# Kernel optimization log

Measured on AMD Instinct MI355X. Metric: run time of the kernel, lower is better.

Reference implementation:

```python
import jax, jax.numpy as jnp
import numpy as np

N, M, D_IN, H1, D, OUT_C = 2048, 128, 352, 512, 256, 13


def _lin_bn_relu(x, w, b, g, be):
    # 1x1 conv == linear over last dim; BN (eval) folded to per-channel affine (g, be)
    return jax.nn.relu(g * (x @ w.T + b) + be)


def _encode(x, wA, bA, gA, beA, wB, bB, gB, beB):
    return _lin_bn_relu(_lin_bn_relu(x, wA, bA, gA, beA), wB, bB, gB, beB)


def setup_inputs() -> dict:
    key = jax.random.key(0)
    ks = iter(jax.random.split(key, 64))

    def wgt(shape, s=0.05):
        return (jax.random.normal(next(ks), shape, jnp.float32) * s)

    def gamma(c):
        return 1.0 + 0.05 * jax.random.normal(next(ks), (c,), jnp.float32)

    inp = {}
    inp['ext_fea'] = jax.random.normal(next(ks), (N, D_IN), jnp.float32)
    inp['lab_fea'] = jax.random.normal(next(ks), (M, D_IN), jnp.float32)
    # convs1: 352->512->256, each Conv1d(1x1)+BN+ReLU
    inp.update(w1a=wgt((H1, D_IN)), b1a=wgt((H1,)), g1a=gamma(H1), be1a=wgt((H1,)))
    inp.update(w1b=wgt((D, H1)), b1b=wgt((D,)), g1b=gamma(D), be1b=wgt((D,)))
    # convs2: same shapes
    inp.update(w2a=wgt((H1, D_IN)), b2a=wgt((H1,)), g2a=gamma(H1), be2a=wgt((H1,)))
    inp.update(w2b=wgt((D, H1)), b2b=wgt((D,)), g2b=gamma(D), be2b=wgt((D,)))
    # wei_conv SharedMLP [256,32,64,256]: three Conv2d(1x1)+BN+ReLU
    inp.update(mw1=wgt((32, D)), mb1=wgt((32,)), mg1=gamma(32), mbe1=wgt((32,)))
    inp.update(mw2=wgt((64, 32)), mb2=wgt((64,)), mg2=gamma(64), mbe2=wgt((64,)))
    inp.update(mw3=wgt((D, 64)), mb3=wgt((D,)), mg3=gamma(D), mbe3=wgt((D,)))
    # fc
    inp.update(fcw=wgt((OUT_C, D)), fcb=wgt((OUT_C,)))
    return inp


def reference(ext_fea, lab_fea,
              w1a, b1a, g1a, be1a, w1b, b1b, g1b, be1b,
              w2a, b2a, g2a, be2a, w2b, b2b, g2b, be2b,
              mw1, mb1, mg1, mbe1, mw2, mb2, mg2, mbe2, mw3, mb3, mg3, mbe3,
              fcw, fcb):
    A = _encode(ext_fea, w1a, b1a, g1a, be1a, w1b, b1b, g1b, be1b)   # [N, 256]
    B = _encode(lab_fea, w2a, b2a, g2a, be2a, w2b, b2b, g2b, be2b)   # [M, 256]
    diff = A[:, None, :] - B[None, :, :]                             # [N, M, 256]
    h = _lin_bn_relu(diff, mw1, mb1, mg1, mbe1)                      # [N, M, 32]
    h = _lin_bn_relu(h, mw2, mb2, mg2, mbe2)                         # [N, M, 64]
    wei = _lin_bn_relu(h, mw3, mb3, mg3, mbe3)                       # [N, M, 256]
    # torch softmax over dim=-1 of [1,256,N,M] == over M == axis 1 here
    wei = jax.nn.softmax(wei, axis=1)
    att = jnp.sum(wei * diff, axis=1)                                # [N, 256]
    return att @ fcw.T + fcb                                         # [N, 13]
```

## Files before the change

### kernel.cpp

```cpp
#include <hip/hip_runtime.h>
#include <stdint.h>


typedef __attribute__((ext_vector_type(4))) float float4_t;
typedef __attribute__((ext_vector_type(4))) float f32x4;
typedef __attribute__((ext_vector_type(8))) short bf16x8;
typedef __attribute__((ext_vector_type(8))) unsigned short ushort8_t;
typedef __attribute__((ext_vector_type(4))) unsigned short ushort4_t;
typedef unsigned short ushort_t;

__device__ __forceinline__ float b2f(unsigned short u) {
  union { unsigned int i; float f; } v; v.i = ((unsigned int)u) << 16; return v.f;
}
__device__ __forceinline__ unsigned short f2b(float f) {
  union { float f; unsigned int i; } v; v.f = f;
  unsigned int x = v.i;
  return (unsigned short)((x + 0x7FFFu + ((x >> 16) & 1u)) >> 16);
}

template<int ISBF>
__device__ __forceinline__ ushort8_t ld8(const void* base, size_t idx) {
  if constexpr (ISBF) {
    return *(const ushort8_t*)((const ushort_t*)base + idx);
  } else {
    const float* p = (const float*)base + idx;
    float4_t v0 = *(const float4_t*)p;
    float4_t v1 = *(const float4_t*)(p + 4);
    ushort8_t u;
    #pragma unroll
    for (int e = 0; e < 4; ++e) { u[e] = f2b(v0[e]); u[4 + e] = f2b(v1[e]); }
    return u;
  }
}

template<int XBF, int WBF, int OUT_BF16>
__global__ __launch_bounds__(256) void enc_mfma(
    const void* __restrict__ XA, const void* __restrict__ WA,
    const float* __restrict__ bA, const float* __restrict__ gA, const float* __restrict__ beA,
    void* __restrict__ YA,
    const void* __restrict__ XB, const void* __restrict__ WB,
    const float* __restrict__ bB, const float* __restrict__ gB, const float* __restrict__ beB,
    void* __restrict__ YB, ushort_t* __restrict__ YBTb,
    int J, int K, int nbxA)
{
  __shared__ ushort_t Xs[2][32][72];
  __shared__ ushort_t Ws[2][32][72];
  const int bx = blockIdx.x, by = blockIdx.y;
  const void* X; const void* W;
  const float *bb, *gg, *bev; void* Y; int i0, isB;
  if (bx < nbxA) { X = XA; W = WA; bb = bA; gg = gA; bev = beA; Y = YA; i0 = bx * 32; isB = 0; }
  else           { X = XB; W = WB; bb = bB; gg = gB; bev = beB; Y = YB; i0 = (bx - nbxA) * 32; isB = 1; }
  const int j0 = by * 32;
  const int tid = threadIdx.x, w = tid >> 6, lane = tid & 63, lg = lane >> 4, lr = lane & 15;
  const int mt = w >> 1, ct = w & 1;
  const int row = tid >> 3, k8 = (tid & 7) * 8;

  f32x4 acc = f32x4{0.f, 0.f, 0.f, 0.f};

  ushort8_t xv = ld8<XBF>(X, (size_t)(i0 + row) * K + k8);
  ushort8_t wv = ld8<WBF>(W, (size_t)(j0 + row) * K + k8);
  for (int kt = 0; kt < K; kt += 64) {
    const int buf = (kt >> 6) & 1;
    *(ushort8_t*)&Xs[buf][row][k8] = xv;
    *(ushort8_t*)&Ws[buf][row][k8] = wv;
    __syncthreads();
    if (kt + 64 < K && kt + 64 + k8 < K) {
      xv = ld8<XBF>(X, (size_t)(i0 + row) * K + kt + 64 + k8);
      wv = ld8<WBF>(W, (size_t)(j0 + row) * K + kt + 64 + k8);
    }
    bf16x8 af0 = *(const bf16x8*)&Xs[buf][mt * 16 + lr][lg * 8];
    bf16x8 bf0 = *(const bf16x8*)&Ws[buf][ct * 16 + lr][lg * 8];
    acc = __builtin_amdgcn_mfma_f32_16x16x32_bf16(af0, bf0, acc, 0, 0, 0);
    if (kt + 32 < K) {
      bf16x8 af1 = *(const bf16x8*)&Xs[buf][mt * 16 + lr][32 + lg * 8];
      bf16x8 bf1 = *(const bf16x8*)&Ws[buf][ct * 16 + lr][32 + lg * 8];
      acc = __builtin_amdgcn_mfma_f32_16x16x32_bf16(af1, bf1, acc, 0, 0, 0);
    }
  }
  const int c = j0 + ct * 16 + lr;
  const float g = gg[c], bv = bb[c], ev = bev[c];
  #pragma unroll
  for (int r = 0; r < 4; ++r) {
    const int rowo = i0 + mt * 16 + 4 * lg + r;
    float t = fmaxf(g * (acc[r] + bv) + ev, 0.f);
    if (OUT_BF16) ((ushort_t*)Y)[(size_t)rowo * J + c] = f2b(t);
    else {
      ((float*)Y)[(size_t)rowo * J + c] = t;
      if (isB && YBTb) YBTb[(size_t)c * 128 + rowo] = f2b(t);
    }
  }
}

__global__ __launch_bounds__(256) void proj32(
    const float* __restrict__ Aenc, const float* __restrict__ Benc,
    const float* __restrict__ mw1, const float* __restrict__ mb1,
    const float* __restrict__ mg1, const float* __restrict__ mbe1,
    float* __restrict__ PA2, float* __restrict__ PB2, int nbxA,
    const float* __restrict__ mw2, const float* __restrict__ mw3,
    ushort_t* __restrict__ mw2b, ushort_t* __restrict__ mw3b)
{
  __shared__ float ps[4][32];
  const int tid = threadIdx.x, bx = blockIdx.x;
  if (bx >= nbxA + 32) {
    const int g = (bx - nbxA - 32) * 256 + tid;
    const float* s; ushort_t* d; int j;
    if (g < 256) { s = mw2; d = mw2b; j = g; }
    else         { s = mw3; d = mw3b; j = g - 256; }
    float4_t v0 = *(const float4_t*)&s[(size_t)j * 8];
    float4_t v1 = *(const float4_t*)&s[(size_t)j * 8 + 4];
    ushort8_t u;
    #pragma unroll
    for (int e = 0; e < 4; ++e) { u[e] = f2b(v0[e]); u[4 + e] = f2b(v1[e]); }
    *(ushort8_t*)&d[(size_t)j * 8] = u;
    return;
  }
  const float* X; float* P; int n0, wb;
  if (bx < nbxA) { X = Aenc; P = PA2; n0 = bx * 4; wb = 1; }
  else           { X = Benc; P = PB2; n0 = (bx - nbxA) * 4; wb = 0; }
  const int k = tid & 31, r = (tid >> 5) & 3, half = tid >> 7;
  const int n = n0 + r;
  const float* xp = &X[(size_t)n * 256 + half * 128];
  const float* wp = &mw1[k * 256 + half * 128];
  float s = 0.f;
  #pragma unroll 8
  for (int q = 0; q < 128; q += 4) {
    float4_t xv = *(const float4_t*)&xp[q];
    float4_t wv = *(const float4_t*)&wp[q];
    #pragma unroll
    for (int e = 0; e < 4; ++e) s = fmaf(xv[e], wv[e], s);
  }
  if (half == 1) ps[r][k] = s;
  __syncthreads();
  if (half == 0) {
    s += ps[r][k];
    P[(size_t)n * 32 + k] = wb ? (mg1[k] * (s + mb1[k]) + mbe1[k]) : (mg1[k] * s);
  }
}

__global__ __launch_bounds__(256, 2) void main_attn(
    const float* __restrict__ PA2, const float* __restrict__ PB2,
    const float* __restrict__ A, const ushort_t* __restrict__ BmTb,
    const ushort_t* __restrict__ mw2b, const float* __restrict__ mb2,
    const float* __restrict__ mg2, const float* __restrict__ mbe2,
    const ushort_t* __restrict__ mw3b, const float* __restrict__ mb3,
    const float* __restrict__ mg3, const float* __restrict__ mbe3,
    const float* __restrict__ fcw, const float* __restrict__ fcb,
    float* __restrict__ outp)
{
  __shared__ __align__(16) char smem[77824];
  const int tid = threadIdx.x;
  const int w = tid >> 6, lane = tid & 63, lg = lane >> 4, lr = lane & 15;
  const int n = blockIdx.x * 4 + w;
  ushort_t* h2s = (ushort_t*)(smem + w * 19456);
  float* attL   = (float*)(smem + w * 19456 + 18432);
  const float LOG2E = 1.4426950408889634f;

  {
    bf16x8 b1[4];
    float g2h[4], b2h[4], e2h[4];
    #pragma unroll
    for (int jt = 0; jt < 4; ++jt) {
      b1[jt] = *(const bf16x8*)&mw2b[(jt * 16 + lr) * 32 + lg * 8];
      const int j = jt * 16 + lr;
      g2h[jt] = mg2[j]; b2h[jt] = mb2[j]; e2h[jt] = mbe2[j];
    }
    const float* pa = &PA2[(size_t)n * 32 + lg * 8];
    float4_t pa0 = *(const float4_t*)pa;
    float4_t pa1 = *(const float4_t*)(pa + 4);
    #pragma unroll
    for (int mt = 0; mt < 8; ++mt) {
      const float* pb = &PB2[(size_t)(mt * 16 + lr) * 32 + lg * 8];
      float4_t pb0 = *(const float4_t*)pb;
      float4_t pb1 = *(const float4_t*)(pb + 4);
      bf16x8 a1;
      #pragma unroll
      for (int e = 0; e < 4; ++e) {
        a1[e]     = (short)f2b(fmaxf(pa0[e] - pb0[e], 0.f));
        a1[4 + e] = (short)f2b(fmaxf(pa1[e] - pb1[e], 0.f));
      }
      f32x4 acc1[4];
      #pragma unroll
      for (int jt = 0; jt < 4; ++jt) acc1[jt] = f32x4{0.f, 0.f, 0.f, 0.f};
      #pragma unroll
      for (int jt = 0; jt < 4; ++jt)
        acc1[jt] = __builtin_amdgcn_mfma_f32_16x16x32_bf16(a1, b1[jt], acc1[jt], 0, 0, 0);
      #pragma unroll
      for (int jt = 0; jt < 4; ++jt)
        #pragma unroll
        for (int r = 0; r < 4; ++r)
          h2s[(mt * 16 + 4 * lg + r) * 72 + jt * 16 + lr] =
              f2b(fmaxf(g2h[jt] * (acc1[jt][r] + b2h[jt]) + e2h[jt], 0.f));
    }
  }

  bf16x8 af0[8], af1[8];
  #pragma unroll
  for (int mt = 0; mt < 8; ++mt) {
    af0[mt] = *(const bf16x8*)&h2s[(mt * 16 + lr) * 72 + lg * 8];
    af1[mt] = *(const bf16x8*)&h2s[(mt * 16 + lr) * 72 + 32 + lg * 8];
  }

  #pragma unroll 4
  for (int ct = 0; ct < 16; ++ct) {
    const int c = ct * 16 + lr;
    bf16x8 bfr0 = *(const bf16x8*)&mw3b[(size_t)c * 64 + lg * 8];
    bf16x8 bfr1 = *(const bf16x8*)&mw3b[(size_t)c * 64 + 32 + lg * 8];
    f32x4 acc[8];
    #pragma unroll
    for (int mt = 0; mt < 8; ++mt) acc[mt] = f32x4{0.f, 0.f, 0.f, 0.f};
    #pragma unroll
    for (int mt = 0; mt < 8; ++mt) {
      acc[mt] = __builtin_amdgcn_mfma_f32_16x16x32_bf16(af0[mt], bfr0, acc[mt], 0, 0, 0);
      acc[mt] = __builtin_amdgcn_mfma_f32_16x16x32_bf16(af1[mt], bfr1, acc[mt], 0, 0, 0);
    }
    const float g = mg3[c];
    const float gs = g * LOG2E;
    const float cs = (g * mb3[c] + mbe3[c]) * LOG2E;
    f32x4 sm4 = f32x4{0.f, 0.f, 0.f, 0.f};
    f32x4 wb4 = f32x4{0.f, 0.f, 0.f, 0.f};
    #pragma unroll
    for (int mt = 0; mt < 8; ++mt) {
      ushort4_t bv4 = *(const ushort4_t*)&BmTb[(size_t)c * 128 + mt * 16 + 4 * lg];
      #pragma unroll
      for (int r = 0; r < 4; ++r) {
        float t = fmaf(gs, acc[mt][r], cs);
        float p = __builtin_amdgcn_exp2f(__builtin_amdgcn_fmed3f(t, 0.f, 80.f));
        sm4[r] += p;
        wb4[r] = fmaf(p, b2f(bv4[r]), wb4[r]);
      }
    }
    float sm = (sm4[0] + sm4[1]) + (sm4[2] + sm4[3]);
    float wb = (wb4[0] + wb4[1]) + (wb4[2] + wb4[3]);
    sm += __shfl_xor(sm, 16, 64);  wb += __shfl_xor(wb, 16, 64);
    sm += __shfl_xor(sm, 32, 64);  wb += __shfl_xor(wb, 32, 64);
    if (lg == 0)
      attL[c] = A[(size_t)n * 256 + c] - wb / sm;
  }

  {
    float4_t av = *(const float4_t*)&attL[lane * 4];
    #pragma unroll
    for (int o = 0; o < 13; ++o) {
      float4_t wv = *(const float4_t*)&fcw[(size_t)o * 256 + lane * 4];
      float s = av[0] * wv[0];
      s = fmaf(av[1], wv[1], s);
      s = fmaf(av[2], wv[2], s);
      s = fmaf(av[3], wv[3], s);
      #pragma unroll
      for (int st = 1; st <= 32; st <<= 1) s += __shfl_xor(s, st, 64);
      if (lane == 0) outp[(size_t)n * 13 + o] = s + fcb[o];
    }
  }
}

extern "C" void kernel_launch(void* const* d_in, const int* in_sizes, int n_in,
                              void* d_out, int out_size, void* d_ws, size_t ws_size,
                              hipStream_t stream)
{
  const float* ext = (const float*)d_in[0];
  const float* lab = (const float*)d_in[1];
  const float* w1a = (const float*)d_in[2];
  const float* b1a = (const float*)d_in[3];
  const float* g1a = (const float*)d_in[4];
  const float* be1a= (const float*)d_in[5];
  const float* w1b = (const float*)d_in[6];
  const float* b1b = (const float*)d_in[7];
  const float* g1b = (const float*)d_in[8];
  const float* be1b= (const float*)d_in[9];
  const float* w2a = (const float*)d_in[10];
  const float* b2a = (const float*)d_in[11];
  const float* g2a = (const float*)d_in[12];
  const float* be2a= (const float*)d_in[13];
  const float* w2b = (const float*)d_in[14];
  const float* b2b = (const float*)d_in[15];
  const float* g2b = (const float*)d_in[16];
  const float* be2b= (const float*)d_in[17];
  const float* mw1 = (const float*)d_in[18];
  const float* mb1 = (const float*)d_in[19];
  const float* mg1 = (const float*)d_in[20];
  const float* mbe1= (const float*)d_in[21];
  const float* mw2 = (const float*)d_in[22];
  const float* mb2 = (const float*)d_in[23];
  const float* mg2 = (const float*)d_in[24];
  const float* mbe2= (const float*)d_in[25];
  const float* mw3 = (const float*)d_in[26];
  const float* mb3 = (const float*)d_in[27];
  const float* mg3 = (const float*)d_in[28];
  const float* mbe3= (const float*)d_in[29];
  const float* fcw = (const float*)d_in[30];
  const float* fcb = (const float*)d_in[31];

  char* ws = (char*)d_ws;
  ushort_t* Y1ab = (ushort_t*)(ws);
  float*    PA2  = (float*)(ws);
  float*    PB2  = (float*)(ws + 262144);
  float*    Aenc = (float*)(ws + (2u << 20));
  char* b5 = ws + (4u << 20);
  ushort_t* mw2b  = (ushort_t*)(b5);
  ushort_t* mw3b  = (ushort_t*)(b5 + 4096);
  ushort_t* Y1bb  = (ushort_t*)(b5 + 36864);
  float*    Benc  = (float*)(b5 + 167936);
  ushort_t* BencTb= (ushort_t*)(b5 + 299008);

  enc_mfma<0, 0, 1><<<dim3(68, 16), 256, 0, stream>>>(
      (const void*)ext, (const void*)w1a, b1a, g1a, be1a, (void*)Y1ab,
      (const void*)lab, (const void*)w2a, b2a, g2a, be2a, (void*)Y1bb,
      (ushort_t*)nullptr, 512, 352, 64);
  enc_mfma<1, 0, 0><<<dim3(68, 8), 256, 0, stream>>>(
      (const void*)Y1ab, (const void*)w1b, b1b, g1b, be1b, (void*)Aenc,
      (const void*)Y1bb, (const void*)w2b, b2b, g2b, be2b, (void*)Benc,
      BencTb, 256, 512, 64);
  proj32<<<553, 256, 0, stream>>>(Aenc, Benc, mw1, mb1, mg1, mbe1, PA2, PB2, 512,
                                  mw2, mw3, mw2b, mw3b);
  main_attn<<<512, 256, 0, stream>>>(PA2, PB2, Aenc, BencTb,
                                     mw2b, mb2, mg2, mbe2, mw3b, mb3, mg3, mbe3,
                                     fcw, fcb, (float*)d_out);
}
```

Measured before the change: 82.47 us.

## Fuse 32-wide projection into second encoder epilogue and drop proj32 kernel

Removes the separate proj32 launch. The mw1 projection is computed in the second encoder kernel's epilogue: each block takes partial dot products over its 32 output channels and accumulates them into zeroed PA2/PB2 buffers with atomicAdd. The bf16 weight conversion moves into extra blocks of the first encoder launch. MFMA priority hints are added in main_attn. The change saves a launch and a reread of Aenc/Benc, but adds a memset, float atomics (nondeterministic summation order) and extra shared memory in the encoder.

Result: slower. 89.40 us (+8.4%).

```diff
diff --git a/kernel.cpp b/kernel.cpp
--- a/kernel.cpp
+++ b/kernel.cpp
@@ -33,7 +33,7 @@
   }
 }
 
-template<int XBF, int WBF, int OUT_BF16>
+template<int XBF, int WBF, int OUT_BF16, int DO_CVT, int DO_PROJ>
 __global__ __launch_bounds__(256) void enc_mfma(
     const void* __restrict__ XA, const void* __restrict__ WA,
     const float* __restrict__ bA, const float* __restrict__ gA, const float* __restrict__ beA,
@@ -41,11 +41,35 @@
     const void* __restrict__ XB, const void* __restrict__ WB,
     const float* __restrict__ bB, const float* __restrict__ gB, const float* __restrict__ beB,
     void* __restrict__ YB, ushort_t* __restrict__ YBTb,
-    int J, int K, int nbxA)
+    int J, int K, int nbxA,
+    const float* __restrict__ mw2, const float* __restrict__ mw3,
+    ushort_t* __restrict__ mw2b, ushort_t* __restrict__ mw3b,
+    const float* __restrict__ mw1, const float* __restrict__ mg1,
+    const float* __restrict__ mb1, const float* __restrict__ mbe1,
+    float* __restrict__ PA2, float* __restrict__ PB2)
 {
   __shared__ ushort_t Xs[2][32][72];
   __shared__ ushort_t Ws[2][32][72];
+  __shared__ float tileT[32][33];
   const int bx = blockIdx.x, by = blockIdx.y;
+
+  if constexpr (DO_CVT) {
+    if (bx >= nbxA + 4) {
+      if (by != 0) return;
+      const int g = (bx - nbxA - 4) * 256 + threadIdx.x;
+      const float* s; ushort_t* d; int j;
+      if (g < 256) { s = mw2; d = mw2b; j = g; }
+      else         { s = mw3; d = mw3b; j = g - 256; }
+      float4_t v0 = *(const float4_t*)&s[(size_t)j * 8];
+      float4_t v1 = *(const float4_t*)&s[(size_t)j * 8 + 4];
+      ushort8_t u;
+      #pragma unroll
+      for (int e = 0; e < 4; ++e) { u[e] = f2b(v0[e]); u[4 + e] = f2b(v1[e]); }
+      *(ushort8_t*)&d[(size_t)j * 8] = u;
+      return;
+    }
+  }
+
   const void* X; const void* W;
   const float *bb, *gg, *bev; void* Y; int i0, isB;
   if (bx < nbxA) { X = XA; W = WA; bb = bA; gg = gA; bev = beA; Y = YA; i0 = bx * 32; isB = 0; }
@@ -79,61 +103,50 @@
   }
   const int c = j0 + ct * 16 + lr;
   const float g = gg[c], bv = bb[c], ev = bev[c];
+  float tv[4];
   #pragma unroll
   for (int r = 0; r < 4; ++r) {
     const int rowo = i0 + mt * 16 + 4 * lg + r;
-    float t = fmaxf(g * (acc[r] + bv) + ev, 0.f);
-    if (OUT_BF16) ((ushort_t*)Y)[(size_t)rowo * J + c] = f2b(t);
+    tv[r] = fmaxf(g * (acc[r] + bv) + ev, 0.f);
+    if (OUT_BF16) ((ushort_t*)Y)[(size_t)rowo * J + c] = f2b(tv[r]);
     else {
-      ((float*)Y)[(size_t)rowo * J + c] = t;
-      if (isB && YBTb) YBTb[(size_t)c * 128 + rowo] = f2b(t);
-    }
-  }
-}
-
-__global__ __launch_bounds__(256) void proj32(
-    const float* __restrict__ Aenc, const float* __restrict__ Benc,
-    const float* __restrict__ mw1, const float* __restrict__ mb1,
-    const float* __restrict__ mg1, const float* __restrict__ mbe1,
-    float* __restrict__ PA2, float* __restrict__ PB2, int nbxA,
-    const float* __restrict__ mw2, const float* __restrict__ mw3,
-    ushort_t* __restrict__ mw2b, ushort_t* __restrict__ mw3b)
-{
-  __shared__ float ps[4][32];
-  const int tid = threadIdx.x, bx = blockIdx.x;
-  if (bx >= nbxA + 32) {
-    const int g = (bx - nbxA - 32) * 256 + tid;
-    const float* s; ushort_t* d; int j;
-    if (g < 256) { s = mw2; d = mw2b; j = g; }
-    else         { s = mw3; d = mw3b; j = g - 256; }
-    float4_t v0 = *(const float4_t*)&s[(size_t)j * 8];
-    float4_t v1 = *(const float4_t*)&s[(size_t)j * 8 + 4];
-    ushort8_t u;
-    #pragma unroll
-    for (int e = 0; e < 4; ++e) { u[e] = f2b(v0[e]); u[4 + e] = f2b(v1[e]); }
-    *(ushort8_t*)&d[(size_t)j * 8] = u;
-    return;
-  }
-  const float* X; float* P; int n0, wb;
-  if (bx < nbxA) { X = Aenc; P = PA2; n0 = bx * 4; wb = 1; }
-  else           { X = Benc; P = PB2; n0 = (bx - nbxA) * 4; wb = 0; }
-  const int k = tid & 31, r = (tid >> 5) & 3, half = tid >> 7;
-  const int n = n0 + r;
-  const float* xp = &X[(size_t)n * 256 + half * 128];
-  const float* wp = &mw1[k * 256 + half * 128];
-  float s = 0.f;
-  #pragma unroll 8
-  for (int q = 0; q < 128; q += 4) {
-    float4_t xv = *(const float4_t*)&xp[q];
-    float4_t wv = *(const float4_t*)&wp[q];
-    #pragma unroll
-    for (int e = 0; e < 4; ++e) s = fmaf(xv[e], wv[e], s);
-  }
-  if (half == 1) ps[r][k] = s;
-  __syncthreads();
-  if (half == 0) {
-    s += ps[r][k];
-    P[(size_t)n * 32 + k] = wb ? (mg1[k] * (s + mb1[k]) + mbe1[k]) : (mg1[k] * s);
+      ((float*)Y)[(size_t)rowo * J + c] = tv[r];
+      if (isB && YBTb) YBTb[(size_t)c * 128 + rowo] = f2b(tv[r]);
+    }
+  }
+
+  if constexpr (DO_PROJ) {
+    #pragma unroll
+    for (int r = 0; r < 4; ++r)
+      tileT[mt * 16 + 4 * lg + r][ct * 16 + lr] = tv[r];
+    __syncthreads();
+    const int rowl = tid >> 3, k0 = (tid & 7) * 4;
+    float s0 = 0.f, s1 = 0.f, s2 = 0.f, s3 = 0.f;
+    #pragma unroll 4
+    for (int cl = 0; cl < 32; cl += 4) {
+      float4_t av = *(const float4_t*)&tileT[rowl][cl];
+      float4_t w0 = *(const float4_t*)&mw1[(size_t)(k0 + 0) * 256 + j0 + cl];
+      float4_t w1 = *(const float4_t*)&mw1[(size_t)(k0 + 1) * 256 + j0 + cl];
+      float4_t w2 = *(const float4_t*)&mw1[(size_t)(k0 + 2) * 256 + j0 + cl];
+      float4_t w3 = *(const float4_t*)&mw1[(size_t)(k0 + 3) * 256 + j0 + cl];
+      #pragma unroll
+      for (int e = 0; e < 4; ++e) {
+        s0 = fmaf(av[e], w0[e], s0);
+        s1 = fmaf(av[e], w1[e], s1);
+        s2 = fmaf(av[e], w2[e], s2);
+        s3 = fmaf(av[e], w3[e], s3);
+      }
+    }
+    const int rowg = i0 + rowl;
+    float* P = isB ? PB2 : PA2;
+    float sv[4] = { s0, s1, s2, s3 };
+    #pragma unroll
+    for (int kk = 0; kk < 4; ++kk) {
+      const int k = k0 + kk;
+      float v = mg1[k] * sv[kk];
+      if (!isB && by == 0) v += mg1[k] * mb1[k] + mbe1[k];
+      atomicAdd(&P[(size_t)rowg * 32 + k], v);
+    }
   }
 }
 
@@ -208,11 +221,13 @@
     f32x4 acc[8];
     #pragma unroll
     for (int mt = 0; mt < 8; ++mt) acc[mt] = f32x4{0.f, 0.f, 0.f, 0.f};
+    __builtin_amdgcn_s_setprio(1);
     #pragma unroll
     for (int mt = 0; mt < 8; ++mt) {
       acc[mt] = __builtin_amdgcn_mfma_f32_16x16x32_bf16(af0[mt], bfr0, acc[mt], 0, 0, 0);
       acc[mt] = __builtin_amdgcn_mfma_f32_16x16x32_bf16(af1[mt], bfr1, acc[mt], 0, 0, 0);
     }
+    __builtin_amdgcn_s_setprio(0);
     const float g = mg3[c];
     const float gs = g * LOG2E;
     const float cs = (g * mb3[c] + mbe3[c]) * LOG2E;
@@ -292,8 +307,6 @@
 
   char* ws = (char*)d_ws;
   ushort_t* Y1ab = (ushort_t*)(ws);
-  float*    PA2  = (float*)(ws);
-  float*    PB2  = (float*)(ws + 262144);
   float*    Aenc = (float*)(ws + (2u << 20));
   char* b5 = ws + (4u << 20);
   ushort_t* mw2b  = (ushort_t*)(b5);
@@ -301,17 +314,25 @@
   ushort_t* Y1bb  = (ushort_t*)(b5 + 36864);
   float*    Benc  = (float*)(b5 + 167936);
   ushort_t* BencTb= (ushort_t*)(b5 + 299008);
-
-  enc_mfma<0, 0, 1><<<dim3(68, 16), 256, 0, stream>>>(
+  float*    PA2   = (float*)(b5 + 364544);
+  float*    PB2   = (float*)(b5 + 626688);
+
+  hipMemsetAsync((void*)PA2, 0, 262144 + 16384, stream);
+  enc_mfma<0, 0, 1, 1, 0><<<dim3(77, 16), 256, 0, stream>>>(
       (const void*)ext, (const void*)w1a, b1a, g1a, be1a, (void*)Y1ab,
       (const void*)lab, (const void*)w2a, b2a, g2a, be2a, (void*)Y1bb,
-      (ushort_t*)nullptr, 512, 352, 64);
-  enc_mfma<1, 0, 0><<<dim3(68, 8), 256, 0, stream>>>(
+      (ushort_t*)nullptr, 512, 352, 64,
+      mw2, mw3, mw2b, mw3b,
+      (const float*)nullptr, (const float*)nullptr,
+      (const float*)nullptr, (const float*)nullptr,
+      (float*)nullptr, (float*)nullptr);
+  enc_mfma<1, 0, 0, 0, 1><<<dim3(68, 8), 256, 0, stream>>>(
       (const void*)Y1ab, (const void*)w1b, b1b, g1b, be1b, (void*)Aenc,
       (const void*)Y1bb, (const void*)w2b, b2b, g2b, be2b, (void*)Benc,
-      BencTb, 256, 512, 64);
-  proj32<<<553, 256, 0, stream>>>(Aenc, Benc, mw1, mb1, mg1, mbe1, PA2, PB2, 512,
-                                  mw2, mw3, mw2b, mw3b);
+      BencTb, 256, 512, 64,
+      (const float*)nullptr, (const float*)nullptr,
+      (ushort_t*)nullptr, (ushort_t*)nullptr,
+      mw1, mg1, mb1, mbe1, PA2, PB2);
   main_attn<<<512, 256, 0, stream>>>(PA2, PB2, Aenc, BencTb,
                                      mw2b, mb2, mg2, mbe2, mw3b, mb3, mg3, mbe3,
                                      fcw, fcb, (float*)d_out);
```
